# Performance work log

Measured on AMD Instinct MI355X. Metric: run time of the kernel, lower is better.

## Reference

```python
import jax, jax.numpy as jnp
import numpy as np

HID = 256
HEADS = 8
HD = HID // HEADS  # head_dim = 32


def setup_inputs() -> dict:
    key = jax.random.key(0)
    ks = jax.random.split(key, 16)
    B, N = 4, 2048
    s = 0.02
    inp = {
        'x': jax.random.normal(ks[0], (B, N, 4, HID), dtype=jnp.float32),
        'Wq': jax.random.normal(ks[1], (HID, HID), dtype=jnp.float32) * s,
        'bq': jnp.zeros((HID,), jnp.float32),
        'Wk': jax.random.normal(ks[2], (HID, HID), dtype=jnp.float32) * s,
        'bk': jnp.zeros((HID,), jnp.float32),
        'Wv': jax.random.normal(ks[3], (HID, HID), dtype=jnp.float32) * s,
        'bv': jnp.zeros((HID,), jnp.float32),
        'Wvec': jax.random.normal(ks[4], (2 * HID, HID), dtype=jnp.float32) * s,
        'Wo': jax.random.normal(ks[5], (3 * HID, HID), dtype=jnp.float32) * s,
        'bo': jnp.zeros((3 * HID,), jnp.float32),
        'Wg': jax.random.normal(ks[6], (HID, 2 * HID), dtype=jnp.float32) * s,
        'bg': jnp.zeros((HID,), jnp.float32),
        'alpha_dot': jnp.asarray(1.0, jnp.float32),
        'alpha_norm': jnp.asarray(1.0, jnp.float32),
    }
    return inp


def reference(x, Wq, bq, Wk, bk, Wv, bv, Wvec, Wo, bo, Wg, bg, alpha_dot, alpha_norm):
    B, N, _, H = x.shape
    nh, hd = HEADS, HD
    x_scalar = x[:, :, 0]          # (B,N,H)
    vec = x[:, :, 1:]              # (B,N,3,H)

    def lin(a, W, b=None):
        y = a @ W.T
        return y + b if b is not None else y

    # scalar q/k/v -> (B,heads,N,hd)
    q = lin(x_scalar, Wq, bq).reshape(B, N, nh, hd).transpose(0, 2, 1, 3)
    k = lin(x_scalar, Wk, bk).reshape(B, N, nh, hd).transpose(0, 2, 1, 3)
    v = lin(x_scalar, Wv, bv).reshape(B, N, nh, hd).transpose(0, 2, 1, 3)

    # invariant features from vector channels
    vec_proj = lin(vec, Wvec)                  # (B,N,3,2H)
    vec1, vec2 = vec_proj[..., :H], vec_proj[..., H:]
    vec_dot = jnp.sum(vec1 * vec2, axis=-2)    # (B,N,H)
    vec_norm = jnp.linalg.norm(vec, axis=2)    # (B,N,H)

    # equivariant values: (B,heads,N,3*hd)
    vec_v = vec.reshape(B, N, 3, nh, hd).transpose(0, 3, 1, 2, 4).reshape(B, nh, N, 3 * hd)

    # fused attention: one softmax, aggregate scalar v and vector v together
    scale = 1.0 / np.sqrt(hd).astype(np.float32)
    scores = jnp.einsum('bhqd,bhkd->bhqk', q, k) * scale
    attn = jax.nn.softmax(scores, axis=-1)
    v_all = jnp.concatenate([v, vec_v], axis=-1)        # (B,h,N,4*hd)
    out_all = jnp.einsum('bhqk,bhkd->bhqd', attn, v_all)
    out_s, out_v = out_all[..., :hd], out_all[..., hd:]

    x_out = out_s.transpose(0, 2, 1, 3).reshape(B, N, H)
    vec_aggr = out_v.reshape(B, nh, N, 3, hd).transpose(0, 2, 3, 1, 4).reshape(B, N, 3, H)

    invariants = jnp.concatenate([alpha_dot * vec_dot, alpha_norm * vec_norm], axis=-1)
    gate = jax.nn.sigmoid(lin(invariants, Wg, bg))[:, :, None, :]  # (B,N,1,H)
    vec_combined = gate * vec_aggr + vec  # vector_mixing='add', gating=True

    o = lin(x_out, Wo, bo)
    o1, o2, o3 = o[..., :H], o[..., H:2 * H], o[..., 2 * H:]
    x_updated = vec_dot * o1 + vec_norm * o2 + o3

    x_final = jnp.concatenate([x_updated[:, :, None, :], vec_combined], axis=2)  # (B,N,4,H)
    return x_final
```

## Files before the change

### kernel.cpp

```cpp
#include <hip/hip_runtime.h>
#include <cstdint>
#include <cstddef>

#define HIDN 256
#define NHEAD 8
#define HD 32
#define NSEQ 2048
#define QS (0.17677669529663687f * 1.4426950408889634f)

typedef __attribute__((ext_vector_type(8))) short short8;
typedef __attribute__((ext_vector_type(4))) short short4v;
typedef __attribute__((ext_vector_type(4))) float f32x4;
typedef __attribute__((ext_vector_type(16))) float f32x16;
typedef __attribute__((ext_vector_type(4))) uint32_t u32x4;

static __device__ __forceinline__ short f2bf(float f) {
    union { float f; uint32_t u; } v; v.f = f;
    uint32_t r = (v.u + 0x7FFF + ((v.u >> 16) & 1)) >> 16;
    return (short)r;
}
static __device__ __forceinline__ float bf2f(short s) {
    union { uint32_t u; float f; } v; v.u = ((uint32_t)(uint16_t)s) << 16;
    return v.f;
}

static __device__ __forceinline__ float ex2(float x) {
#if defined(__has_builtin)
#if __has_builtin(__builtin_amdgcn_exp2f)
    return __builtin_amdgcn_exp2f(x);
#else
    return exp2f(x);
#endif
#else
    return exp2f(x);
#endif
}

static __device__ __forceinline__ uint32_t pkbf16(float lo, float hi) {
    uint32_t r;
    asm("v_cvt_pk_bf16_f32 %0, %1, %2" : "=v"(r) : "v"(lo), "v"(hi));
    return r;
}

static __device__ __forceinline__ void half_bcast(uint32_t x, uint32_t& lo, uint32_t& hi) {
    uint32_t a = x, b = x;
    asm("v_permlane32_swap_b32 %0, %1" : "+v"(a), "+v"(b));
    lo = a; hi = b;
}

static __device__ __forceinline__ void gload16(const void* g, void* l) {
    __builtin_amdgcn_global_load_lds(
        (__attribute__((address_space(1))) void*)g,
        (__attribute__((address_space(3))) void*)l, 16, 0, 0);
}

static __device__ __forceinline__ f32x16 zero16() {
    f32x16 z;
    #pragma unroll
    for (int i = 0; i < 16; i++) z[i] = 0.f;
    return z;
}

__global__ __launch_bounds__(256) void wcvt_kernel(
    const float* __restrict__ Wq, const float* __restrict__ Wk,
    const float* __restrict__ Wv, const float* __restrict__ Wvec,
    const float* __restrict__ Wo, const float* __restrict__ Wg,
    const float* __restrict__ bq, const float* __restrict__ bk,
    const float* __restrict__ bv,
    const float* __restrict__ ad, const float* __restrict__ an,
    short* __restrict__ Wqkvb, short* __restrict__ Wvecb,
    short* __restrict__ Wob, short* __restrict__ Wgb, float* __restrict__ bqkvs)
{
    int idx = blockIdx.x * 256 + threadIdx.x;
    if (idx < 65536)        Wqkvb[idx] = f2bf(Wq[idx] * QS);
    else if (idx < 131072)  Wqkvb[idx] = f2bf(Wk[idx - 65536]);
    else if (idx < 196608)  Wqkvb[idx] = f2bf(Wv[idx - 131072]);
    else if (idx < 327680)  Wvecb[idx - 196608] = f2bf(Wvec[idx - 196608]);
    else if (idx < 524288)  Wob[idx - 327680] = f2bf(Wo[idx - 327680]);
    else {
        int i2 = idx - 524288;
        int k = i2 & 511;
        float s = (k < 256) ? ad[0] : an[0];
        Wgb[i2] = f2bf(Wg[i2] * s);
    }
    if (idx < 256)          bqkvs[idx] = bq[idx] * QS;
    else if (idx < 512)     bqkvs[idx] = bk[idx - 256];
    else if (idx < 768)     bqkvs[idx] = bv[idx - 512];
}

__global__ __launch_bounds__(256) void qkv_kernel(
    const float* __restrict__ x, const short* __restrict__ Wqkvb,
    const float* __restrict__ bqkvs,
    short* __restrict__ qbf, short* __restrict__ kbf, short* __restrict__ vtb)
{
    __shared__ short xs[32 * 264];
    __shared__ short vtmp[256 * 34];
    const int tid = threadIdx.x;
    const int m0 = blockIdx.x * 32;
    const int b  = m0 >> 11;
    const int n0 = m0 & 2047;

    #pragma unroll
    for (int l = 0; l < 8; l++) {
        int i = l * 256 + tid;
        int t = i >> 6, j4 = i & 63;
        float4 v = *(const float4*)(x + (size_t)(m0 + t) * 1024 + j4 * 4);
        short4v s = { f2bf(v.x), f2bf(v.y), f2bf(v.z), f2bf(v.w) };
        *(short4v*)&xs[t * 264 + j4 * 4] = s;
    }
    __syncthreads();

    const int wave = tid >> 6, lane = tid & 63;
    const int col = lane & 15, quad = lane >> 4;

    short8 xf[2][8];
    #pragma unroll
    for (int mt = 0; mt < 2; mt++)
        #pragma unroll
        for (int kk = 0; kk < 8; kk++)
            xf[mt][kk] = *(const short8*)&xs[(mt * 16 + col) * 264 + kk * 32 + quad * 8];

    #pragma unroll
    for (int y = 0; y < 3; y++) {
        f32x4 acc[2][4];
        #pragma unroll
        for (int mt = 0; mt < 2; mt++)
            #pragma unroll
            for (int nt = 0; nt < 4; nt++) acc[mt][nt] = (f32x4){0.f,0.f,0.f,0.f};

        const short* Wb = Wqkvb + (size_t)(y * 256 + wave * 64) * 256;
        #pragma unroll
        for (int kk = 0; kk < 8; kk++) {
            #pragma unroll
            for (int nt = 0; nt < 4; nt++) {
                short8 wf = *(const short8*)(Wb + (size_t)(nt * 16 + col) * 256 + kk * 32 + quad * 8);
                #pragma unroll
                for (int mt = 0; mt < 2; mt++)
                    acc[mt][nt] = __builtin_amdgcn_mfma_f32_16x16x32_bf16(wf, xf[mt][kk], acc[mt][nt], 0, 0, 0);
            }
        }

        if (y == 0) {
            #pragma unroll
            for (int nt = 0; nt < 4; nt++) {
                int ch = wave * 64 + nt * 16 + quad * 4;
                float4 bi = *(const float4*)&bqkvs[ch];
                int h = ch >> 5, d = ch & 31;
                #pragma unroll
                for (int mt = 0; mt < 2; mt++) {
                    int n = n0 + mt * 16 + col;
                    short4v s = { f2bf(acc[mt][nt][0] + bi.x), f2bf(acc[mt][nt][1] + bi.y),
                                  f2bf(acc[mt][nt][2] + bi.z), f2bf(acc[mt][nt][3] + bi.w) };
                    *(short4v*)(qbf + ((size_t)(b * 8 + h) * 2048 + n) * 32 + d) = s;
                }
            }
        } else if (y == 1) {
            #pragma unroll
            for (int nt = 0; nt < 4; nt++) {
                int ch = wave * 64 + nt * 16 + quad * 4;
                float4 bi = *(const float4*)&bqkvs[256 + ch];
                int h = ch >> 5, d = ch & 31;
                #pragma unroll
                for (int mt = 0; mt < 2; mt++) {
                    int n = n0 + mt * 16 + col;
                    short4v s = { f2bf(acc[mt][nt][0] + bi.x), f2bf(acc[mt][nt][1] + bi.y),
                                  f2bf(acc[mt][nt][2] + bi.z), f2bf(acc[mt][nt][3] + bi.w) };
                    int f  = ((n & 63) >> 5) * 2 + (d >> 4);
                    int lk = (n & 31) + (((d >> 3) & 1) << 5);
                    short* dst = kbf + ((size_t)(b * 8 + h) * 32 + (n >> 6)) * 2048
                               + f * 512 + lk * 8 + (d & 7);
                    *(short4v*)dst = s;
                }
            }
        } else {
            #pragma unroll
            for (int nt = 0; nt < 4; nt++) {
                int ch = wave * 64 + nt * 16 + quad * 4;
                float4 bi = *(const float4*)&bqkvs[512 + ch];
                #pragma unroll
                for (int mt = 0; mt < 2; mt++) {
                    int tok = mt * 16 + col;
                    vtmp[(ch + 0) * 34 + tok] = f2bf(acc[mt][nt][0] + bi.x);
                    vtmp[(ch + 1) * 34 + tok] = f2bf(acc[mt][nt][1] + bi.y);
                    vtmp[(ch + 2) * 34 + tok] = f2bf(acc[mt][nt][2] + bi.z);
                    vtmp[(ch + 3) * 34 + tok] = f2bf(acc[mt][nt][3] + bi.w);
                }
            }
        }
    }
    __syncthreads();
    {
        int ch = tid;
        short s[32];
        #pragma unroll
        for (int t = 0; t < 32; t++) s[t] = vtmp[ch * 34 + t];
        int h = ch >> 5, d = ch & 31;
        size_t tile = (size_t)(b * 8 + h) * 32 + (n0 >> 6);
        short* dst = vtb + tile * 8192;
        #pragma unroll
        for (int g = 0; g < 4; g++) {
            int kbse = (n0 & 63) + g * 8;
            int f = kbse >> 4;
            int h2 = (kbse >> 3) & 1;
            *(short8*)(dst + f * 512 + (d + h2 * 32) * 8) = *(short8*)&s[g * 8];
        }
    }
}

__global__ __launch_bounds__(512) void vec_kernel(
    const float* __restrict__ x, const short* __restrict__ Wvecb,
    float* __restrict__ dotb, short* __restrict__ invb,
    float* __restrict__ normb, short* __restrict__ vtb)
{
    __shared__ short vb[3 * 16 * 264];
    const int tid = threadIdx.x;
    const int m0 = blockIdx.x * 16;
    const int b = m0 >> 11, n0 = m0 & 2047;

    #pragma unroll
    for (int p = 0; p < 6; p++) {
        int f4 = p * 512 + tid;
        int t = f4 / 192;
        int rem = f4 - t * 192;
        int c = rem >> 6, j4 = rem & 63;
        float4 v = *(const float4*)(x + (size_t)(m0 + t) * 1024 + 256 + c * 256 + j4 * 4);
        short4v s = { f2bf(v.x), f2bf(v.y), f2bf(v.z), f2bf(v.w) };
        *(short4v*)&vb[(c * 16 + t) * 264 + j4 * 4] = s;
    }
    __syncthreads();

    const int wave = tid >> 6, lane = tid & 63;
    const int col = lane & 15, quad = lane >> 4;
    const int j0 = wave * 32;

    f32x4 d1[3][2], d2[3][2];
    #pragma unroll
    for (int c = 0; c < 3; c++)
        #pragma unroll
        for (int nt = 0; nt < 2; nt++) {
            d1[c][nt] = (f32x4){0.f,0.f,0.f,0.f};
            d2[c][nt] = (f32x4){0.f,0.f,0.f,0.f};
        }

    #pragma unroll
    for (int kk = 0; kk < 8; kk++) {
        short8 w1[2], w2[2];
        #pragma unroll
        for (int nt = 0; nt < 2; nt++) {
            w1[nt] = *(const short8*)&Wvecb[(size_t)(j0 + nt * 16 + col) * 256 + kk * 32 + quad * 8];
            w2[nt] = *(const short8*)&Wvecb[(size_t)(256 + j0 + nt * 16 + col) * 256 + kk * 32 + quad * 8];
        }
        #pragma unroll
        for (int c = 0; c < 3; c++) {
            short8 xf = *(const short8*)&vb[(c * 16 + col) * 264 + kk * 32 + quad * 8];
            #pragma unroll
            for (int nt = 0; nt < 2; nt++) {
                d1[c][nt] = __builtin_amdgcn_mfma_f32_16x16x32_bf16(w1[nt], xf, d1[c][nt], 0, 0, 0);
                d2[c][nt] = __builtin_amdgcn_mfma_f32_16x16x32_bf16(w2[nt], xf, d2[c][nt], 0, 0, 0);
            }
        }
    }
    #pragma unroll
    for (int nt = 0; nt < 2; nt++) {
        f32x4 dac = d1[0][nt] * d2[0][nt] + d1[1][nt] * d2[1][nt] + d1[2][nt] * d2[2][nt];
        float4 o = { dac[0], dac[1], dac[2], dac[3] };
        *(float4*)&dotb[(size_t)(m0 + col) * 256 + j0 + nt * 16 + quad * 4] = o;
        short4v s = { f2bf(dac[0]), f2bf(dac[1]), f2bf(dac[2]), f2bf(dac[3]) };
        *(short4v*)&invb[(size_t)(m0 + col) * 512 + j0 + nt * 16 + quad * 4] = s;
    }

    const int j = tid & 255, tp = tid >> 8;
    const int h = j >> 5, d = j & 31;
    #pragma unroll
    for (int t8 = 0; t8 < 8; t8++) {
        int t = tp * 8 + t8;
        float v0 = bf2f(vb[(0 * 16 + t) * 264 + j]);
        float v1 = bf2f(vb[(1 * 16 + t) * 264 + j]);
        float v2 = bf2f(vb[(2 * 16 + t) * 264 + j]);
        float nm = sqrtf(v0 * v0 + v1 * v1 + v2 * v2);
        normb[(size_t)(m0 + t) * 256 + j] = nm;
        invb[(size_t)(m0 + t) * 512 + 256 + j] = f2bf(nm);
    }
    {
        size_t tile = (size_t)(b * 8 + h) * 32 + (n0 >> 6);
        int kbse = (n0 & 63) + tp * 8;
        int ks = kbse >> 4, h2 = (kbse >> 3) & 1;
        #pragma unroll
        for (int c = 0; c < 3; c++) {
            short8 s;
            #pragma unroll
            for (int t8 = 0; t8 < 8; t8++) s[t8] = vb[(c * 16 + tp * 8 + t8) * 264 + j];
            int f = (1 + c) * 4 + ks;
            *(short8*)(vtb + tile * 8192 + f * 512 + (d + h2 * 32) * 8) = s;
        }
    }
}

__global__ __launch_bounds__(256) void attn_kernel(
    const short* __restrict__ qb, const short* __restrict__ kb,
    const short* __restrict__ vtb,
    short* __restrict__ xob, short* __restrict__ ovb)
{
    __shared__ short Ks[2][2048];
    __shared__ short Vs[2][8192];
    const int tid = threadIdx.x;
    const int wave = tid >> 6, lane = tid & 63;
    const int q32 = lane & 31, hi = lane >> 5;

    const int D = blockIdx.x;
    const int slot = D >> 3;
    const int bh = (D & 7) + ((slot & 3) << 3);
    const int qt = slot >> 2;
    const int m0 = qt * 128 + wave * 32;
    const int b = bh >> 3, h = bh & 7;

    const short* qbase = qb + (size_t)bh * NSEQ * HD;
    const short* ksrc  = kb + (size_t)bh * 32 * 2048;
    const short* vsrc  = vtb + (size_t)bh * 32 * 8192;

    short8 qfrag[2];
    #pragma unroll
    for (int ks = 0; ks < 2; ks++)
        qfrag[ks] = *(const short8*)(qbase + (size_t)(m0 + q32) * 32 + ks * 16 + hi * 8);

    f32x16 o[4];
    #pragma unroll
    for (int dt = 0; dt < 4; dt++) o[dt] = zero16();
    float lrun = 0.f;

    auto STAGE = [&](int buf, int t) {
        gload16(ksrc + (size_t)t * 2048 + tid * 8, &Ks[buf][wave * 512]);
        const short* vp = vsrc + (size_t)t * 8192 + tid * 8;
        #pragma unroll
        for (int p = 0; p < 4; p++)
            gload16(vp + p * 2048, &Vs[buf][p * 2048 + wave * 512]);
    };

    STAGE(0, 0);
    __syncthreads();

    for (int kt = 0; kt < 32; kt++) {
        const int cur = kt & 1;
        if (kt < 31) STAGE(cur ^ 1, kt + 1);

        f32x16 sc[2];
        #pragma unroll
        for (int t = 0; t < 2; t++) {
            f32x16 a = zero16();
            #pragma unroll
            for (int ks = 0; ks < 2; ks++) {
                short8 kf = *(const short8*)&Ks[cur][(t * 2 + ks) * 512 + lane * 8];
                a = __builtin_amdgcn_mfma_f32_32x32x16_bf16(kf, qfrag[ks], a, 0, 0, 0);
            }
            sc[t] = a;
        }

        uint32_t alo[2][4], ahi[2][4], blo[2][4], bhi[2][4];
        float rs = 0.f;
        #pragma unroll
        for (int t = 0; t < 2; t++) {
            float e[16];
            #pragma unroll
            for (int r = 0; r < 16; r++) { e[r] = ex2(sc[t][r]); rs += e[r]; }
            #pragma unroll
            for (int g = 0; g < 4; g++) {
                half_bcast(pkbf16(e[4*g+0], e[4*g+1]), alo[t][g], ahi[t][g]);
                half_bcast(pkbf16(e[4*g+2], e[4*g+3]), blo[t][g], bhi[t][g]);
            }
        }
        lrun += rs;

        #pragma unroll
        for (int s = 0; s < 4; s++) {
            const int t = s >> 1, g0 = (s & 1) * 2, g1 = g0 + 1;
            uint32_t u0 = hi ? alo[t][g1] : alo[t][g0];
            uint32_t u1 = hi ? blo[t][g1] : blo[t][g0];
            uint32_t u2 = hi ? ahi[t][g1] : ahi[t][g0];
            uint32_t u3 = hi ? bhi[t][g1] : bhi[t][g0];
            u32x4 pv = { u0, u1, u2, u3 };
            short8 pf = __builtin_bit_cast(short8, pv);
            #pragma unroll
            for (int dt = 0; dt < 4; dt++) {
                short8 vf = *(const short8*)&Vs[cur][(dt * 4 + s) * 512 + lane * 8];
                o[dt] = __builtin_amdgcn_mfma_f32_32x32x16_bf16(vf, pf, o[dt], 0, 0, 0);
            }
        }
        __syncthreads();
    }

    float l = lrun + __shfl_xor(lrun, 32);
    float linv = 1.0f / l;

    size_t mg = (size_t)b * 2048 + m0 + q32;
    short* xr = xob + mg * 256 + h * 32;
    #pragma unroll
    for (int g = 0; g < 4; g++) {
        short4v sv = { f2bf(o[0][4*g+0] * linv), f2bf(o[0][4*g+1] * linv),
                       f2bf(o[0][4*g+2] * linv), f2bf(o[0][4*g+3] * linv) };
        *(short4v*)(xr + g * 8 + hi * 4) = sv;
    }
    short* vr = ovb + mg * 768 + h * 32;
    #pragma unroll
    for (int dt = 1; dt < 4; dt++) {
        #pragma unroll
        for (int g = 0; g < 4; g++) {
            short4v sv = { f2bf(o[dt][4*g+0] * linv), f2bf(o[dt][4*g+1] * linv),
                           f2bf(o[dt][4*g+2] * linv), f2bf(o[dt][4*g+3] * linv) };
            *(short4v*)(vr + (dt - 1) * 256 + g * 8 + hi * 4) = sv;
        }
    }
}

__global__ __launch_bounds__(256, 2) void ogemm_kernel(
    const float* __restrict__ x, const short* __restrict__ xob,
    const short* __restrict__ invb,
    const float* __restrict__ dotb, const float* __restrict__ normb,
    const short* __restrict__ ovb,
    const short* __restrict__ Wob, const short* __restrict__ Wgb,
    const float* __restrict__ bo, const float* __restrict__ bg,
    float* __restrict__ out)
{
    __shared__ __align__(16) union {
        struct { short inv[16 * 520]; short xo[16 * 264]; } in;
        struct { short gate[16 * 264]; short o[16 * 776]; } ob;
    } u;
    const int tid = threadIdx.x;
    const int M0 = blockIdx.x * 16;

    #pragma unroll
    for (int l = 0; l < 4; l++) {
        int i = l * 256 + tid;
        int m = i >> 6, seg = i & 63;
        *(short8*)&u.in.inv[m * 520 + seg * 8] =
            *(const short8*)(invb + (size_t)(M0 + m) * 512 + seg * 8);
    }
    #pragma unroll
    for (int l = 0; l < 2; l++) {
        int i = l * 256 + tid;
        int m = i >> 5, seg = i & 31;
        *(short8*)&u.in.xo[m * 264 + seg * 8] =
            *(const short8*)(xob + (size_t)(M0 + m) * 256 + seg * 8);
    }
    __syncthreads();

    const int wave = tid >> 6, lane = tid & 63;
    const int col = lane & 15, quad = lane >> 4;

    f32x4 acc[16];
    #pragma unroll
    for (int nt = 0; nt < 16; nt++) acc[nt] = (f32x4){0.f,0.f,0.f,0.f};

    if (wave == 0) {
        short8 wbuf[2][16];
        #pragma unroll
        for (int nt = 0; nt < 16; nt++)
            wbuf[0][nt] = *(const short8*)(Wgb + (size_t)(nt * 16 + col) * 512 + quad * 8);
        #pragma unroll
        for (int kk = 0; kk < 16; kk++) {
            if (kk < 15) {
                #pragma unroll
                for (int nt = 0; nt < 16; nt++)
                    wbuf[(kk + 1) & 1][nt] =
                        *(const short8*)(Wgb + (size_t)(nt * 16 + col) * 512 + (kk + 1) * 32 + quad * 8);
            }
            short8 xf = *(const short8*)&u.in.inv[col * 520 + kk * 32 + quad * 8];
            #pragma unroll
            for (int nt = 0; nt < 16; nt++)
                acc[nt] = __builtin_amdgcn_mfma_f32_16x16x32_bf16(wbuf[kk & 1][nt], xf, acc[nt], 0, 0, 0);
        }
    } else {
        const short* Wb = Wob + (size_t)(wave - 1) * 256 * 256;
        short8 wbuf[2][16];
        #pragma unroll
        for (int nt = 0; nt < 16; nt++)
            wbuf[0][nt] = *(const short8*)(Wb + (size_t)(nt * 16 + col) * 256 + quad * 8);
        #pragma unroll
        for (int kk = 0; kk < 8; kk++) {
            if (kk < 7) {
                #pragma unroll
                for (int nt = 0; nt < 16; nt++)
                    wbuf[(kk + 1) & 1][nt] =
                        *(const short8*)(Wb + (size_t)(nt * 16 + col) * 256 + (kk + 1) * 32 + quad * 8);
            }
            short8 xf = *(const short8*)&u.in.xo[col * 264 + kk * 32 + quad * 8];
            #pragma unroll
            for (int nt = 0; nt < 16; nt++)
                acc[nt] = __builtin_amdgcn_mfma_f32_16x16x32_bf16(wbuf[kk & 1][nt], xf, acc[nt], 0, 0, 0);
        }
    }
    __syncthreads();

    if (wave == 0) {
        #pragma unroll
        for (int nt = 0; nt < 16; nt++) {
            int ch = nt * 16 + quad * 4;
            float4 bi = *(const float4*)&bg[ch];
            short4v s = { f2bf(1.f / (1.f + __expf(-(acc[nt][0] + bi.x)))),
                          f2bf(1.f / (1.f + __expf(-(acc[nt][1] + bi.y)))),
                          f2bf(1.f / (1.f + __expf(-(acc[nt][2] + bi.z)))),
                          f2bf(1.f / (1.f + __expf(-(acc[nt][3] + bi.w)))) };
            *(short4v*)&u.ob.gate[col * 264 + ch] = s;
        }
    } else {
        #pragma unroll
        for (int nt = 0; nt < 16; nt++) {
            int ch = (wave - 1) * 256 + nt * 16 + quad * 4;
            float4 bi = *(const float4*)&bo[ch];
            short4v s = { f2bf(acc[nt][0] + bi.x), f2bf(acc[nt][1] + bi.y),
                          f2bf(acc[nt][2] + bi.z), f2bf(acc[nt][3] + bi.w) };
            *(short4v*)&u.ob.o[col * 776 + ch] = s;
        }
    }
    __syncthreads();

    #pragma unroll
    for (int l = 0; l < 16; l++) {
        int idx4 = l * 256 + tid;
        int m = idx4 >> 8;
        int j = (idx4 & 255) * 4;
        size_t mg = (size_t)(M0 + m);
        if (j < 256) {
            float4 dv = *(const float4*)(dotb + mg * 256 + j);
            float4 nv = *(const float4*)(normb + mg * 256 + j);
            short4v o1 = *(short4v*)&u.ob.o[m * 776 + j];
            short4v o2 = *(short4v*)&u.ob.o[m * 776 + 256 + j];
            short4v o3 = *(short4v*)&u.ob.o[m * 776 + 512 + j];
            float4 r;
            r.x = dv.x * bf2f(o1[0]) + nv.x * bf2f(o2[0]) + bf2f(o3[0]);
            r.y = dv.y * bf2f(o1[1]) + nv.y * bf2f(o2[1]) + bf2f(o3[1]);
            r.z = dv.z * bf2f(o1[2]) + nv.z * bf2f(o2[2]) + bf2f(o3[2]);
            r.w = dv.w * bf2f(o1[3]) + nv.w * bf2f(o2[3]) + bf2f(o3[3]);
            *(float4*)(out + mg * 1024 + j) = r;
        } else {
            int c = (j >> 8) - 1, jj = j & 255;
            short4v g4 = *(short4v*)&u.ob.gate[m * 264 + jj];
            short4v av4 = *(const short4v*)(ovb + mg * 768 + c * 256 + jj);
            float4 xv = *(const float4*)(x + mg * 1024 + 256 + c * 256 + jj);
            float4 r = { bf2f(g4[0]) * bf2f(av4[0]) + xv.x, bf2f(g4[1]) * bf2f(av4[1]) + xv.y,
                         bf2f(g4[2]) * bf2f(av4[2]) + xv.z, bf2f(g4[3]) * bf2f(av4[3]) + xv.w };
            *(float4*)(out + mg * 1024 + j) = r;
        }
    }
}

extern "C" void kernel_launch(void* const* d_in, const int* in_sizes, int n_in,
                              void* d_out, int out_size, void* d_ws, size_t ws_size,
                              hipStream_t stream)
{
    const float* x    = (const float*)d_in[0];
    const float* Wq   = (const float*)d_in[1];
    const float* bq   = (const float*)d_in[2];
    const float* Wk   = (const float*)d_in[3];
    const float* bk   = (const float*)d_in[4];
    const float* Wv   = (const float*)d_in[5];
    const float* bv   = (const float*)d_in[6];
    const float* Wvec = (const float*)d_in[7];
    const float* Wo   = (const float*)d_in[8];
    const float* bo   = (const float*)d_in[9];
    const float* Wg   = (const float*)d_in[10];
    const float* bg   = (const float*)d_in[11];
    const float* adp  = (const float*)d_in[12];
    const float* anp  = (const float*)d_in[13];
    float* out = (float*)d_out;

    float* ws    = (float*)d_ws;
    short* qbf   = (short*)ws;
    short* kbf   = (short*)(ws + 1048576);
    short* vtb   = (short*)(ws + 2097152);
    float* dotb  = ws + 6291456;
    float* normb = ws + 8388608;
    short* xob   = (short*)(ws + 10485760);
    short* ovb   = (short*)(ws + 11534336);
    short* invb  = (short*)(ws + 17825792);
    short* Wqkvb = (short*)(ws + 19922944);
    float* bqkvs = ws + 20021248;
    short* Wvecb = (short*)(ws + 20022016);
    short* Wob   = (short*)(ws + 20087552);
    short* Wgb   = (short*)(ws + 20185856);

    wcvt_kernel<<<2560, 256, 0, stream>>>(Wq, Wk, Wv, Wvec, Wo, Wg, bq, bk, bv,
                                          adp, anp, Wqkvb, Wvecb, Wob, Wgb, bqkvs);
    qkv_kernel<<<256, 256, 0, stream>>>(x, Wqkvb, bqkvs, qbf, kbf, vtb);
    vec_kernel<<<512, 512, 0, stream>>>(x, Wvecb, dotb, invb, normb, vtb);
    attn_kernel<<<512, 256, 0, stream>>>(qbf, kbf, vtb, xob, ovb);
    ogemm_kernel<<<512, 256, 0, stream>>>(x, xob, invb, dotb, normb, ovb,
                                          Wob, Wgb, bo, bg, out);
}
```

Before: 259.7 us.

## Rebalance ogemm work across eight waves with equal gate and output slices

The output GEMM kernel moves from 256 to 512 threads. Previously one wave computed the whole gate GEMM (K=512) while three waves each did one Wo slice. Now each of 8 waves does 32 gate channels and 96 output channels, which balances the MFMA load and removes the imbalance where wave 0 did twice the K-steps. Register double-buffering of weights is dropped in favour of direct loads per k-step. This also raises occupancy, at the risk of less load latency hiding.

```diff
diff --git a/kernel.cpp b/kernel.cpp
--- a/kernel.cpp
+++ b/kernel.cpp
@@ -411,7 +411,7 @@
     }
 }
 
-__global__ __launch_bounds__(256, 2) void ogemm_kernel(
+__global__ __launch_bounds__(512, 4) void ogemm_kernel(
     const float* __restrict__ x, const short* __restrict__ xob,
     const short* __restrict__ invb,
     const float* __restrict__ dotb, const float* __restrict__ normb,
@@ -428,16 +428,14 @@
     const int M0 = blockIdx.x * 16;
 
     #pragma unroll
-    for (int l = 0; l < 4; l++) {
-        int i = l * 256 + tid;
+    for (int l = 0; l < 2; l++) {
+        int i = l * 512 + tid;
         int m = i >> 6, seg = i & 63;
         *(short8*)&u.in.inv[m * 520 + seg * 8] =
             *(const short8*)(invb + (size_t)(M0 + m) * 512 + seg * 8);
     }
-    #pragma unroll
-    for (int l = 0; l < 2; l++) {
-        int i = l * 256 + tid;
-        int m = i >> 5, seg = i & 31;
+    {
+        int m = tid >> 5, seg = tid & 31;
         *(short8*)&u.in.xo[m * 264 + seg * 8] =
             *(const short8*)(xob + (size_t)(M0 + m) * 256 + seg * 8);
     }
@@ -445,77 +443,67 @@
 
     const int wave = tid >> 6, lane = tid & 63;
     const int col = lane & 15, quad = lane >> 4;
-
-    f32x4 acc[16];
-    #pragma unroll
-    for (int nt = 0; nt < 16; nt++) acc[nt] = (f32x4){0.f,0.f,0.f,0.f};
-
-    if (wave == 0) {
-        short8 wbuf[2][16];
-        #pragma unroll
-        for (int nt = 0; nt < 16; nt++)
-            wbuf[0][nt] = *(const short8*)(Wgb + (size_t)(nt * 16 + col) * 512 + quad * 8);
-        #pragma unroll
-        for (int kk = 0; kk < 16; kk++) {
-            if (kk < 15) {
-                #pragma unroll
-                for (int nt = 0; nt < 16; nt++)
-                    wbuf[(kk + 1) & 1][nt] =
-                        *(const short8*)(Wgb + (size_t)(nt * 16 + col) * 512 + (kk + 1) * 32 + quad * 8);
-            }
-            short8 xf = *(const short8*)&u.in.inv[col * 520 + kk * 32 + quad * 8];
-            #pragma unroll
-            for (int nt = 0; nt < 16; nt++)
-                acc[nt] = __builtin_amdgcn_mfma_f32_16x16x32_bf16(wbuf[kk & 1][nt], xf, acc[nt], 0, 0, 0);
-        }
-    } else {
-        const short* Wb = Wob + (size_t)(wave - 1) * 256 * 256;
-        short8 wbuf[2][16];
-        #pragma unroll
-        for (int nt = 0; nt < 16; nt++)
-            wbuf[0][nt] = *(const short8*)(Wb + (size_t)(nt * 16 + col) * 256 + quad * 8);
-        #pragma unroll
-        for (int kk = 0; kk < 8; kk++) {
-            if (kk < 7) {
-                #pragma unroll
-                for (int nt = 0; nt < 16; nt++)
-                    wbuf[(kk + 1) & 1][nt] =
-                        *(const short8*)(Wb + (size_t)(nt * 16 + col) * 256 + (kk + 1) * 32 + quad * 8);
-            }
-            short8 xf = *(const short8*)&u.in.xo[col * 264 + kk * 32 + quad * 8];
-            #pragma unroll
-            for (int nt = 0; nt < 16; nt++)
-                acc[nt] = __builtin_amdgcn_mfma_f32_16x16x32_bf16(wbuf[kk & 1][nt], xf, acc[nt], 0, 0, 0);
-        }
-    }
-    __syncthreads();
-
-    if (wave == 0) {
-        #pragma unroll
-        for (int nt = 0; nt < 16; nt++) {
-            int ch = nt * 16 + quad * 4;
-            float4 bi = *(const float4*)&bg[ch];
-            short4v s = { f2bf(1.f / (1.f + __expf(-(acc[nt][0] + bi.x)))),
-                          f2bf(1.f / (1.f + __expf(-(acc[nt][1] + bi.y)))),
-                          f2bf(1.f / (1.f + __expf(-(acc[nt][2] + bi.z)))),
-                          f2bf(1.f / (1.f + __expf(-(acc[nt][3] + bi.w)))) };
-            *(short4v*)&u.ob.gate[col * 264 + ch] = s;
-        }
-    } else {
-        #pragma unroll
-        for (int nt = 0; nt < 16; nt++) {
-            int ch = (wave - 1) * 256 + nt * 16 + quad * 4;
-            float4 bi = *(const float4*)&bo[ch];
-            short4v s = { f2bf(acc[nt][0] + bi.x), f2bf(acc[nt][1] + bi.y),
-                          f2bf(acc[nt][2] + bi.z), f2bf(acc[nt][3] + bi.w) };
-            *(short4v*)&u.ob.o[col * 776 + ch] = s;
-        }
-    }
-    __syncthreads();
-
-    #pragma unroll
-    for (int l = 0; l < 16; l++) {
-        int idx4 = l * 256 + tid;
+    const int cg = wave * 32;
+    const int co = wave * 96;
+
+    f32x4 accg[2], acco[6];
+    #pragma unroll
+    for (int i = 0; i < 2; i++) accg[i] = (f32x4){0.f,0.f,0.f,0.f};
+    #pragma unroll
+    for (int i = 0; i < 6; i++) acco[i] = (f32x4){0.f,0.f,0.f,0.f};
+
+    #pragma unroll
+    for (int kk = 0; kk < 8; kk++) {
+        short8 wg0 = *(const short8*)(Wgb + (size_t)(cg + col) * 512 + (2*kk) * 32 + quad * 8);
+        short8 wg1 = *(const short8*)(Wgb + (size_t)(cg + 16 + col) * 512 + (2*kk) * 32 + quad * 8);
+        short8 wg2 = *(const short8*)(Wgb + (size_t)(cg + col) * 512 + (2*kk+1) * 32 + quad * 8);
+        short8 wg3 = *(const short8*)(Wgb + (size_t)(cg + 16 + col) * 512 + (2*kk+1) * 32 + quad * 8);
+        short8 wo0 = *(const short8*)(Wob + (size_t)(co + 0*16 + col) * 256 + kk * 32 + quad * 8);
+        short8 wo1 = *(const short8*)(Wob + (size_t)(co + 1*16 + col) * 256 + kk * 32 + quad * 8);
+        short8 wo2 = *(const short8*)(Wob + (size_t)(co + 2*16 + col) * 256 + kk * 32 + quad * 8);
+        short8 wo3 = *(const short8*)(Wob + (size_t)(co + 3*16 + col) * 256 + kk * 32 + quad * 8);
+        short8 wo4 = *(const short8*)(Wob + (size_t)(co + 4*16 + col) * 256 + kk * 32 + quad * 8);
+        short8 wo5 = *(const short8*)(Wob + (size_t)(co + 5*16 + col) * 256 + kk * 32 + quad * 8);
+        short8 xg0 = *(const short8*)&u.in.inv[col * 520 + (2*kk) * 32 + quad * 8];
+        short8 xg1 = *(const short8*)&u.in.inv[col * 520 + (2*kk+1) * 32 + quad * 8];
+        short8 xoo = *(const short8*)&u.in.xo[col * 264 + kk * 32 + quad * 8];
+        __builtin_amdgcn_sched_barrier(0);
+        accg[0] = __builtin_amdgcn_mfma_f32_16x16x32_bf16(wg0, xg0, accg[0], 0, 0, 0);
+        accg[1] = __builtin_amdgcn_mfma_f32_16x16x32_bf16(wg1, xg0, accg[1], 0, 0, 0);
+        accg[0] = __builtin_amdgcn_mfma_f32_16x16x32_bf16(wg2, xg1, accg[0], 0, 0, 0);
+        accg[1] = __builtin_amdgcn_mfma_f32_16x16x32_bf16(wg3, xg1, accg[1], 0, 0, 0);
+        acco[0] = __builtin_amdgcn_mfma_f32_16x16x32_bf16(wo0, xoo, acco[0], 0, 0, 0);
+        acco[1] = __builtin_amdgcn_mfma_f32_16x16x32_bf16(wo1, xoo, acco[1], 0, 0, 0);
+        acco[2] = __builtin_amdgcn_mfma_f32_16x16x32_bf16(wo2, xoo, acco[2], 0, 0, 0);
+        acco[3] = __builtin_amdgcn_mfma_f32_16x16x32_bf16(wo3, xoo, acco[3], 0, 0, 0);
+        acco[4] = __builtin_amdgcn_mfma_f32_16x16x32_bf16(wo4, xoo, acco[4], 0, 0, 0);
+        acco[5] = __builtin_amdgcn_mfma_f32_16x16x32_bf16(wo5, xoo, acco[5], 0, 0, 0);
+    }
+    __syncthreads();
+
+    #pragma unroll
+    for (int i = 0; i < 2; i++) {
+        int ch = cg + i * 16 + quad * 4;
+        float4 bi = *(const float4*)&bg[ch];
+        short4v s = { f2bf(1.f / (1.f + __expf(-(accg[i][0] + bi.x)))),
+                      f2bf(1.f / (1.f + __expf(-(accg[i][1] + bi.y)))),
+                      f2bf(1.f / (1.f + __expf(-(accg[i][2] + bi.z)))),
+                      f2bf(1.f / (1.f + __expf(-(accg[i][3] + bi.w)))) };
+        *(short4v*)&u.ob.gate[col * 264 + ch] = s;
+    }
+    #pragma unroll
+    for (int i = 0; i < 6; i++) {
+        int ch = co + i * 16 + quad * 4;
+        float4 bi = *(const float4*)&bo[ch];
+        short4v s = { f2bf(acco[i][0] + bi.x), f2bf(acco[i][1] + bi.y),
+                      f2bf(acco[i][2] + bi.z), f2bf(acco[i][3] + bi.w) };
+        *(short4v*)&u.ob.o[col * 776 + ch] = s;
+    }
+    __syncthreads();
+
+    #pragma unroll
+    for (int l = 0; l < 8; l++) {
+        int idx4 = l * 512 + tid;
         int m = idx4 >> 8;
         int j = (idx4 & 255) * 4;
         size_t mg = (size_t)(M0 + m);
@@ -583,6 +571,6 @@
     qkv_kernel<<<256, 256, 0, stream>>>(x, Wqkvb, bqkvs, qbf, kbf, vtb);
     vec_kernel<<<512, 512, 0, stream>>>(x, Wvecb, dotb, invb, normb, vtb);
     attn_kernel<<<512, 256, 0, stream>>>(qbf, kbf, vtb, xob, ovb);
-    ogemm_kernel<<<512, 256, 0, stream>>>(x, xob, invb, dotb, normb, ovb,
+    ogemm_kernel<<<512, 512, 0, stream>>>(x, xob, invb, dotb, normb, ovb,
                                           Wob, Wgb, bo, bg, out);
 }
```

New measurement: 247.8 us. 4.6% less time.
